# Optimization experiments

Measured on AMD Instinct MI355X. Metric: run time of the kernel, lower is better.

The kernel has to match this reference:

```python
import jax, jax.numpy as jnp
import numpy as np

NUM_SPEAKERS = 8192  # static stand-in for labels.max()+1
MARGIN = 0.2
EPS = 1e-12  # torch F.normalize default eps


def _l2_normalize(x, axis=1):
    norm = jnp.linalg.norm(x, axis=axis, keepdims=True)
    return x / jnp.maximum(norm, EPS)


def setup_inputs() -> dict:
    key = jax.random.key(0)
    k1, k2 = jax.random.split(key)
    embeddings = jax.random.normal(k1, (8192, 256), dtype=jnp.float32)
    labels = jax.random.randint(k2, (8192,), 0, NUM_SPEAKERS, dtype=jnp.int32)
    return {"embeddings": embeddings, "labels": labels}


def reference(embeddings, labels):
    # Normalize embeddings: [B, D]
    e = _l2_normalize(embeddings, axis=1)
    B = e.shape[0]

    # Scatter-mean prototypes per speaker (replaces the python for-loop):
    sums = jax.ops.segment_sum(e, labels, num_segments=NUM_SPEAKERS)          # [S, D]
    counts = jax.ops.segment_sum(jnp.ones((B,), e.dtype), labels,
                                 num_segments=NUM_SPEAKERS)                    # [S]
    protos = sums / jnp.maximum(counts, 1.0)[:, None]  # zero rows stay zero like torch skip
    protos = _l2_normalize(protos, axis=1)

    # Cosine similarity: [B, S]
    cos_sim = jnp.matmul(e, protos.T)

    # Positive similarity at target column: [B]
    positive_sim = jnp.take_along_axis(cos_sim, labels[:, None].astype(jnp.int32), axis=1)[:, 0]

    # Faithful to original: subtract margin on the diagonal (requires B == S)
    cos_sim_m = cos_sim - MARGIN * jnp.eye(NUM_SPEAKERS, dtype=cos_sim.dtype)
    negative_sim = jnp.max(cos_sim_m, axis=1)

    loss = jnp.mean(jax.nn.relu(negative_sim - positive_sim + MARGIN))
    return loss
```

## Files before the change

### kernel.cpp

```cpp
#include <hip/hip_runtime.h>
#include <hip/hip_bf16.h>

typedef __attribute__((ext_vector_type(8))) short short8;
typedef __attribute__((ext_vector_type(4))) float f32x4;

#define B_ROWS 8192
#define DIM 256
#define CS 8
#define NT 16
#define NSLICE (CS * 2)
#define MARGIN_F 0.2f
#define BUCKET_CAP 32

#define WAITV(n) asm volatile("s_waitcnt vmcnt(" #n ")" ::: "memory")

__device__ __forceinline__ unsigned short f2bf(float x) {
  unsigned int u = __float_as_uint(x);
  unsigned int r = (u + 0x7fffu + ((u >> 16) & 1u)) >> 16;
  return (unsigned short)r;
}
__device__ __forceinline__ float bf2f(unsigned short h) {
  return __uint_as_float(((unsigned int)h) << 16);
}

__device__ __forceinline__ void gload_lds16(const void* g, void* l) {
  __builtin_amdgcn_global_load_lds(
      (const __attribute__((address_space(1))) unsigned int*)g,
      (__attribute__((address_space(3))) unsigned int*)l, 16, 0, 0);
}

__global__ __launch_bounds__(256) void k_norm_index(
    const float* __restrict__ emb, const int* __restrict__ labels,
    unsigned short* __restrict__ ebf, int* __restrict__ cursor,
    int* __restrict__ bucket, float* __restrict__ out) {
  if (blockIdx.x == 0 && threadIdx.x == 0) out[0] = 0.f;
  int wid = threadIdx.x >> 6, lane = threadIdx.x & 63;
  int row = blockIdx.x * 4 + wid;
  const float4 v = *reinterpret_cast<const float4*>(emb + row * DIM + lane * 4);
  float ss = v.x * v.x + v.y * v.y + v.z * v.z + v.w * v.w;
#pragma unroll
  for (int off = 32; off > 0; off >>= 1) ss += __shfl_xor(ss, off);
  float scale = 1.0f / fmaxf(sqrtf(ss), 1e-12f);
  ushort4 ob;
  ob.x = f2bf(v.x * scale); ob.y = f2bf(v.y * scale);
  ob.z = f2bf(v.z * scale); ob.w = f2bf(v.w * scale);
  *reinterpret_cast<ushort4*>(ebf + row * DIM + lane * 4) = ob;
  if (lane == 0) {
    int lab = labels[row];
    int slot = atomicAdd(cursor + lab, 1);
    if (slot < BUCKET_CAP) bucket[lab * BUCKET_CAP + slot] = row;
  }
}

__global__ __launch_bounds__(256) void k_protos_gather(
    const unsigned short* __restrict__ ebf, const int* __restrict__ cursor,
    const int* __restrict__ bucket, unsigned short* __restrict__ pfrag,
    float* __restrict__ pos) {
  int wid = threadIdx.x >> 6, lane = threadIdx.x & 63;
  int p = blockIdx.x * 4 + wid;
  int c = cursor[p];
  if (c > BUCKET_CAP) c = BUCKET_CAP;
  float a0 = 0.f, a1 = 0.f, a2 = 0.f, a3 = 0.f;
  for (int k = 0; k < c; ++k) {
    int row = bucket[p * BUCKET_CAP + k];
    ushort4 ev = *reinterpret_cast<const ushort4*>(ebf + row * DIM + lane * 4);
    a0 += bf2f(ev.x); a1 += bf2f(ev.y); a2 += bf2f(ev.z); a3 += bf2f(ev.w);
  }
  float ss = a0 * a0 + a1 * a1 + a2 * a2 + a3 * a3;
#pragma unroll
  for (int off = 32; off > 0; off >>= 1) ss += __shfl_xor(ss, off);
  float scale = 1.0f / fmaxf(sqrtf(ss), 1e-12f);
  ushort4 ob;
  ob.x = f2bf(a0 * scale); ob.y = f2bf(a1 * scale);
  ob.z = f2bf(a2 * scale); ob.w = f2bf(a3 * scale);
  int addr = (p >> 6) * 16384 + ((((p >> 4) & 3) * 8 + (lane >> 3)) * 512) +
             ((((lane >> 1) & 3) * 16 + (p & 15)) * 8) + ((lane & 1) * 4);
  *reinterpret_cast<ushort4*>(pfrag + addr) = ob;
  float p0 = bf2f(ob.x), p1 = bf2f(ob.y), p2 = bf2f(ob.z), p3 = bf2f(ob.w);
  for (int k = 0; k < c; ++k) {
    int row = bucket[p * BUCKET_CAP + k];
    ushort4 ev = *reinterpret_cast<const ushort4*>(ebf + row * DIM + lane * 4);
    float d = bf2f(ev.x) * p0 + bf2f(ev.y) * p1 + bf2f(ev.z) * p2 +
              bf2f(ev.w) * p3;
#pragma unroll
    for (int off = 32; off > 0; off >>= 1) d += __shfl_xor(d, off);
    if (lane == 0) pos[row] = d;
  }
}

__global__ __attribute__((amdgpu_flat_work_group_size(512, 512)))
__attribute__((amdgpu_waves_per_eu(2, 2))) void k_gemm_negmax(
    const unsigned short* __restrict__ E, const unsigned short* __restrict__ PF,
    float* __restrict__ negp) {
  extern __shared__ unsigned short smb[];
  const int tid = threadIdx.x;
  const int lane = tid & 63, wid = tid >> 6;
  const int l16 = lane & 15, lk = lane >> 4;
  const int wr = (wid >> 1) * 64;
  const int wch = wid & 1;
  const int rowBase = blockIdx.x * 256;
  const int colBase0 = blockIdx.y * 1024;
  const int tile0 = blockIdx.y * NT;

  auto stageB = [&](int buf, int tile) {
#pragma unroll
    for (int it = 0; it < 4; ++it) {
      int c = it * 8 + wid;
      gload_lds16(PF + tile * 16384 + c * 512 + lane * 8,
                  &smb[buf * 16384 + c * 512 + lane * 8]);
    }
  };

  stageB(0, tile0);
  stageB(1, tile0 + 1);
  stageB(2, tile0 + 2);

  short8 areg[4][8];
#pragma unroll
  for (int m = 0; m < 4; ++m)
#pragma unroll
    for (int ks = 0; ks < 8; ++ks)
      areg[m][ks] = *reinterpret_cast<const short8*>(
          E + (rowBase + wr + m * 16 + l16) * DIM + ks * 32 + lk * 8);

  float rmax[4][4];
#pragma unroll
  for (int m = 0; m < 4; ++m)
#pragma unroll
    for (int r = 0; r < 4; ++r) rmax[m][r] = -3.0e38f;

  WAITV(0);
  __builtin_amdgcn_s_barrier();

  auto body = [&](int ct) {
    const unsigned short* bs = &smb[(ct & 3) * 16384];
    f32x4 acc[4][2] = {};
#pragma unroll
    for (int ks = 0; ks < 8; ++ks) {
      short8 b[2];
#pragma unroll
      for (int n = 0; n < 2; ++n)
        b[n] = *reinterpret_cast<const short8*>(
            bs + ((wch * 2 + n) * 8 + ks) * 512 + lane * 8);
#pragma unroll
      for (int m = 0; m < 4; ++m)
#pragma unroll
        for (int n = 0; n < 2; ++n)
          acc[m][n] = __builtin_amdgcn_mfma_f32_16x16x32_bf16(
              areg[m][ks], b[n], acc[m][n], 0, 0, 0);
    }
    const int colT = colBase0 + ct * 64 + wch * 32;
#pragma unroll
    for (int m = 0; m < 4; ++m) {
      int growb = rowBase + wr + m * 16 + lk * 4;
#pragma unroll
      for (int n = 0; n < 2; ++n) {
        int gcol = colT + n * 16 + l16;
#pragma unroll
        for (int r = 0; r < 4; ++r) {
          float v = acc[m][n][r];
          if (growb + r == gcol) v -= MARGIN_F;
          rmax[m][r] = fmaxf(rmax[m][r], v);
        }
      }
    }
  };

  for (int ct = 0; ct < NT - 3; ++ct) {
    body(ct);
    stageB((ct + 3) & 3, tile0 + ct + 3);
    WAITV(8);
    __builtin_amdgcn_s_barrier();
  }
  body(13);
  WAITV(4);
  __builtin_amdgcn_s_barrier();
  body(14);
  WAITV(0);
  __builtin_amdgcn_s_barrier();
  body(15);

  const int slice = blockIdx.y * 2 + wch;
#pragma unroll
  for (int m = 0; m < 4; ++m) {
#pragma unroll
    for (int r = 0; r < 4; ++r) {
      float v = rmax[m][r];
      v = fmaxf(v, __shfl_xor(v, 1));
      v = fmaxf(v, __shfl_xor(v, 2));
      v = fmaxf(v, __shfl_xor(v, 4));
      v = fmaxf(v, __shfl_xor(v, 8));
      if (l16 == 0) {
        int grow = rowBase + wr + m * 16 + lk * 4 + r;
        negp[slice * B_ROWS + grow] = v;
      }
    }
  }
}

__global__ __launch_bounds__(256) void k_loss_part(
    const float* __restrict__ negp, const float* __restrict__ pos,
    float* __restrict__ out) {
  int i = blockIdx.x * 256 + threadIdx.x;
  float n = negp[i];
#pragma unroll
  for (int s = 1; s < NSLICE; ++s) n = fmaxf(n, negp[s * B_ROWS + i]);
  float t = fmaxf(n - pos[i] + MARGIN_F, 0.f);
#pragma unroll
  for (int off = 32; off > 0; off >>= 1) t += __shfl_xor(t, off);
  __shared__ float red[4];
  if ((threadIdx.x & 63) == 0) red[threadIdx.x >> 6] = t;
  __syncthreads();
  if (threadIdx.x == 0)
    atomicAdd(out, (red[0] + red[1] + red[2] + red[3]) * (1.0f / B_ROWS));
}

extern "C" void kernel_launch(void* const* d_in, const int* in_sizes, int n_in,
                              void* d_out, int out_size, void* d_ws, size_t ws_size,
                              hipStream_t stream) {
  const float* emb = (const float*)d_in[0];
  const int* labels = (const int*)d_in[1];

  char* ws = (char*)d_ws;
  int* cursor = (int*)ws;
  int* bucket = (int*)(ws + 32 * 1024);
  unsigned short* ebf =
      (unsigned short*)(ws + 32 * 1024 + 1024 * 1024);
  unsigned short* pfrag =
      (unsigned short*)(ws + 32 * 1024 + 5 * 1024 * 1024);
  float* pos = (float*)(ws + 32 * 1024 + 9 * 1024 * 1024);
  float* negp = (float*)(ws + 64 * 1024 + 9 * 1024 * 1024);

  hipMemsetAsync(cursor, 0, 32 * 1024, stream);
  k_norm_index<<<B_ROWS / 4, 256, 0, stream>>>(emb, labels, ebf, cursor, bucket,
                                               (float*)d_out);
  k_protos_gather<<<B_ROWS / 4, 256, 0, stream>>>(ebf, cursor, bucket, pfrag, pos);
  hipFuncSetAttribute((const void*)k_gemm_negmax,
                      hipFuncAttributeMaxDynamicSharedMemorySize, 131072);
  k_gemm_negmax<<<dim3(32, CS), 512, 131072, stream>>>(ebf, pfrag, negp);
  k_loss_part<<<32, 256, 0, stream>>>(negp, pos, (float*)d_out);
}
```

Baseline: 105.9 us.

## Fuse positive-sim extraction and final loss reduction into GEMM kernel

The positive similarity is now picked from the GEMM accumulators by comparing each column with the row's label, which removes the second gather pass in the prototype kernel. The separate loss kernel is removed: the last GEMM block to finish, found with an atomic counter, does the final max over slices, the hinge and the mean. This saves one launch and some redundant memory traffic. In exchange the GEMM epilogue does extra compare/select work, and the final reduction runs serially in a single block.

```diff
diff --git a/kernel.cpp b/kernel.cpp
--- a/kernel.cpp
+++ b/kernel.cpp
@@ -32,8 +32,7 @@
 __global__ __launch_bounds__(256) void k_norm_index(
     const float* __restrict__ emb, const int* __restrict__ labels,
     unsigned short* __restrict__ ebf, int* __restrict__ cursor,
-    int* __restrict__ bucket, float* __restrict__ out) {
-  if (blockIdx.x == 0 && threadIdx.x == 0) out[0] = 0.f;
+    int* __restrict__ bucket) {
   int wid = threadIdx.x >> 6, lane = threadIdx.x & 63;
   int row = blockIdx.x * 4 + wid;
   const float4 v = *reinterpret_cast<const float4*>(emb + row * DIM + lane * 4);
@@ -54,8 +53,7 @@
 
 __global__ __launch_bounds__(256) void k_protos_gather(
     const unsigned short* __restrict__ ebf, const int* __restrict__ cursor,
-    const int* __restrict__ bucket, unsigned short* __restrict__ pfrag,
-    float* __restrict__ pos) {
+    const int* __restrict__ bucket, unsigned short* __restrict__ pfrag) {
   int wid = threadIdx.x >> 6, lane = threadIdx.x & 63;
   int p = blockIdx.x * 4 + wid;
   int c = cursor[p];
@@ -76,22 +74,14 @@
   int addr = (p >> 6) * 16384 + ((((p >> 4) & 3) * 8 + (lane >> 3)) * 512) +
              ((((lane >> 1) & 3) * 16 + (p & 15)) * 8) + ((lane & 1) * 4);
   *reinterpret_cast<ushort4*>(pfrag + addr) = ob;
-  float p0 = bf2f(ob.x), p1 = bf2f(ob.y), p2 = bf2f(ob.z), p3 = bf2f(ob.w);
-  for (int k = 0; k < c; ++k) {
-    int row = bucket[p * BUCKET_CAP + k];
-    ushort4 ev = *reinterpret_cast<const ushort4*>(ebf + row * DIM + lane * 4);
-    float d = bf2f(ev.x) * p0 + bf2f(ev.y) * p1 + bf2f(ev.z) * p2 +
-              bf2f(ev.w) * p3;
-#pragma unroll
-    for (int off = 32; off > 0; off >>= 1) d += __shfl_xor(d, off);
-    if (lane == 0) pos[row] = d;
-  }
 }
 
 __global__ __attribute__((amdgpu_flat_work_group_size(512, 512)))
 __attribute__((amdgpu_waves_per_eu(2, 2))) void k_gemm_negmax(
     const unsigned short* __restrict__ E, const unsigned short* __restrict__ PF,
-    float* __restrict__ negp) {
+    const int* __restrict__ labels, float* __restrict__ negp,
+    float* __restrict__ pos, int* __restrict__ counter,
+    float* __restrict__ out) {
   extern __shared__ unsigned short smb[];
   const int tid = threadIdx.x;
   const int lane = tid & 63, wid = tid >> 6;
@@ -123,11 +113,21 @@
       areg[m][ks] = *reinterpret_cast<const short8*>(
           E + (rowBase + wr + m * 16 + l16) * DIM + ks * 32 + lk * 8);
 
-  float rmax[4][4];
+  int labv[4][4];
 #pragma unroll
   for (int m = 0; m < 4; ++m)
 #pragma unroll
-    for (int r = 0; r < 4; ++r) rmax[m][r] = -3.0e38f;
+    for (int r = 0; r < 4; ++r)
+      labv[m][r] = labels[rowBase + wr + m * 16 + lk * 4 + r];
+
+  float rmax[4][4], posreg[4][4];
+#pragma unroll
+  for (int m = 0; m < 4; ++m)
+#pragma unroll
+    for (int r = 0; r < 4; ++r) {
+      rmax[m][r] = -3.0e38f;
+      posreg[m][r] = -3.0e38f;
+    }
 
   WAITV(0);
   __builtin_amdgcn_s_barrier();
@@ -159,6 +159,7 @@
 #pragma unroll
         for (int r = 0; r < 4; ++r) {
           float v = acc[m][n][r];
+          posreg[m][r] = (gcol == labv[m][r]) ? v : posreg[m][r];
           if (growb + r == gcol) v -= MARGIN_F;
           rmax[m][r] = fmaxf(rmax[m][r], v);
         }
@@ -190,29 +191,41 @@
       v = fmaxf(v, __shfl_xor(v, 2));
       v = fmaxf(v, __shfl_xor(v, 4));
       v = fmaxf(v, __shfl_xor(v, 8));
-      if (l16 == 0) {
-        int grow = rowBase + wr + m * 16 + lk * 4 + r;
-        negp[slice * B_ROWS + grow] = v;
-      }
-    }
-  }
-}
-
-__global__ __launch_bounds__(256) void k_loss_part(
-    const float* __restrict__ negp, const float* __restrict__ pos,
-    float* __restrict__ out) {
-  int i = blockIdx.x * 256 + threadIdx.x;
-  float n = negp[i];
-#pragma unroll
-  for (int s = 1; s < NSLICE; ++s) n = fmaxf(n, negp[s * B_ROWS + i]);
-  float t = fmaxf(n - pos[i] + MARGIN_F, 0.f);
-#pragma unroll
-  for (int off = 32; off > 0; off >>= 1) t += __shfl_xor(t, off);
-  __shared__ float red[4];
-  if ((threadIdx.x & 63) == 0) red[threadIdx.x >> 6] = t;
+      int grow = rowBase + wr + m * 16 + lk * 4 + r;
+      if (l16 == 0) negp[slice * B_ROWS + grow] = v;
+      if (posreg[m][r] > -1.0e38f) pos[grow] = posreg[m][r];
+    }
+  }
+
+  __threadfence();
   __syncthreads();
-  if (threadIdx.x == 0)
-    atomicAdd(out, (red[0] + red[1] + red[2] + red[3]) * (1.0f / B_ROWS));
+  __shared__ int lastFlag;
+  if (tid == 0) {
+    int done = atomicAdd(counter, 1);
+    lastFlag = (done == (int)(gridDim.x * gridDim.y) - 1);
+  }
+  __syncthreads();
+  if (lastFlag) {
+    __threadfence();
+    float s = 0.f;
+    for (int i = tid; i < B_ROWS; i += 512) {
+      float n = negp[i];
+#pragma unroll
+      for (int sl = 1; sl < NSLICE; ++sl) n = fmaxf(n, negp[sl * B_ROWS + i]);
+      s += fmaxf(n - pos[i] + MARGIN_F, 0.f);
+    }
+#pragma unroll
+    for (int off = 32; off > 0; off >>= 1) s += __shfl_xor(s, off);
+    __shared__ float red[8];
+    if (lane == 0) red[wid] = s;
+    __syncthreads();
+    if (tid == 0) {
+      float t = 0.f;
+#pragma unroll
+      for (int w = 0; w < 8; ++w) t += red[w];
+      out[0] = t * (1.0f / B_ROWS);
+    }
+  }
 }
 
 extern "C" void kernel_launch(void* const* d_in, const int* in_sizes, int n_in,
@@ -223,20 +236,20 @@
 
   char* ws = (char*)d_ws;
   int* cursor = (int*)ws;
-  int* bucket = (int*)(ws + 32 * 1024);
+  int* counter = (int*)(ws + 32 * 1024);
+  int* bucket = (int*)(ws + 64 * 1024);
   unsigned short* ebf =
-      (unsigned short*)(ws + 32 * 1024 + 1024 * 1024);
+      (unsigned short*)(ws + 64 * 1024 + 1024 * 1024);
   unsigned short* pfrag =
-      (unsigned short*)(ws + 32 * 1024 + 5 * 1024 * 1024);
-  float* pos = (float*)(ws + 32 * 1024 + 9 * 1024 * 1024);
-  float* negp = (float*)(ws + 64 * 1024 + 9 * 1024 * 1024);
-
-  hipMemsetAsync(cursor, 0, 32 * 1024, stream);
-  k_norm_index<<<B_ROWS / 4, 256, 0, stream>>>(emb, labels, ebf, cursor, bucket,
-                                               (float*)d_out);
-  k_protos_gather<<<B_ROWS / 4, 256, 0, stream>>>(ebf, cursor, bucket, pfrag, pos);
+      (unsigned short*)(ws + 64 * 1024 + 5 * 1024 * 1024);
+  float* pos = (float*)(ws + 64 * 1024 + 9 * 1024 * 1024);
+  float* negp = (float*)(ws + 128 * 1024 + 9 * 1024 * 1024);
+
+  hipMemsetAsync(cursor, 0, 32 * 1024 + 64, stream);
+  k_norm_index<<<B_ROWS / 4, 256, 0, stream>>>(emb, labels, ebf, cursor, bucket);
+  k_protos_gather<<<B_ROWS / 4, 256, 0, stream>>>(ebf, cursor, bucket, pfrag);
   hipFuncSetAttribute((const void*)k_gemm_negmax,
                       hipFuncAttributeMaxDynamicSharedMemorySize, 131072);
-  k_gemm_negmax<<<dim3(32, CS), 512, 131072, stream>>>(ebf, pfrag, negp);
-  k_loss_part<<<32, 256, 0, stream>>>(negp, pos, (float*)d_out);
-}
+  k_gemm_negmax<<<dim3(32, CS), 512, 131072, stream>>>(
+      ebf, pfrag, labels, negp, pos, counter, (float*)d_out);
+}
```

Result: slower. 191.2 us (+80.6%).
